# Optimization experiments

Measured on AMD Instinct MI355X. Metric: run time of the kernel, lower is better.

The kernel has to match this reference:

```python
import jax, jax.numpy as jnp
import numpy as np

GRID = 32
N_NODES = GRID * GRID          # 1024
PATCH = 1
C_IN = 3
NODE_F = C_IN * PATCH * PATCH  # 3
HID = 256
N_CLASSES = 10


def _build_norm_adj():
    # 5-point grid stencil + self loops, symmetrically normalized: D^-1/2 A D^-1/2
    adj = np.zeros((N_NODES, N_NODES), dtype=np.float32)
    idx = np.arange(N_NODES)
    i, j = idx // GRID, idx % GRID
    adj[idx, idx] = 1.0
    for di, dj in [(-1, 0), (1, 0), (0, -1), (0, 1)]:
        ni, nj = i + di, j + dj
        ok = (ni >= 0) & (ni < GRID) & (nj >= 0) & (nj < GRID)
        adj[idx[ok], (ni * GRID + nj)[ok]] = 1.0
    deg = adj.sum(axis=1)
    dis = np.where(deg > 0, deg ** -0.5, 0.0).astype(np.float32)
    return jnp.asarray(dis[:, None] * adj * dis[None, :])


def _image_to_graph(x):
    # [B,C,H,W] -> [B, grid, patch, grid, patch] blocks -> [B, N, C*patch^2]
    B = x.shape[0]
    x = x.reshape(B, C_IN, GRID, PATCH, GRID, PATCH)
    x = jnp.transpose(x, (0, 2, 4, 1, 3, 5))
    return x.reshape(B, N_NODES, NODE_F)


def setup_inputs() -> dict:
    key = jax.random.key(0)
    ks = jax.random.split(key, 10)
    s = 0.05
    return {
        "x": jax.random.normal(ks[0], (256, 3, 32, 32), dtype=jnp.float32),
        "W1": jax.random.normal(ks[1], (HID, NODE_F), dtype=jnp.float32) * s,
        "b1": jnp.zeros((HID,), dtype=jnp.float32),
        "W2": jax.random.normal(ks[2], (HID, HID), dtype=jnp.float32) * s,
        "b2": jnp.zeros((HID,), dtype=jnp.float32),
        "W3": jax.random.normal(ks[3], (HID // 2, HID), dtype=jnp.float32) * s,
        "b3": jnp.zeros((HID // 2,), dtype=jnp.float32),
        "Wc": jax.random.normal(ks[4], (N_CLASSES, N_NODES * (HID // 2)), dtype=jnp.float32) * s,
        "bc": jnp.zeros((N_CLASSES,), dtype=jnp.float32),
        "adj": _build_norm_adj(),
    }


def _gc(h, W, b, adj):
    # Linear, then fixed-adjacency aggregation, then ReLU
    h = jnp.einsum('bnf,hf->bnh', h, W) + b
    h = jnp.einsum('mn,bnh->bmh', adj, h)
    return jax.nn.relu(h)


def reference(x, W1, b1, W2, b2, W3, b3, Wc, bc, adj):
    h = _image_to_graph(x)                 # [B, N, 3]
    h = _gc(h, W1, b1, adj)                # [B, N, 256]
    h = _gc(h, W2, b2, adj)                # [B, N, 256]
    h = _gc(h, W3, b3, adj)                # [B, N, 128]
    h = h.reshape(h.shape[0], -1)          # [B, N*128]
    return h @ Wc.T + bc                   # [B, 10]
```

## Files before the change

### kernel.cpp

```cpp
#include <hip/hip_runtime.h>
#include <stdint.h>

#define N_NODES 1024
#define NCLS 10
#define KDIM 131072

typedef unsigned short u16;
typedef __bf16 bf16x8 __attribute__((ext_vector_type(8)));
typedef float f32x4 __attribute__((ext_vector_type(4)));
typedef float f32x2 __attribute__((ext_vector_type(2)));

__device__ __forceinline__ float b2f_lo(uint32_t u) {
  union { float f; uint32_t u; } v; v.u = u << 16; return v.f;
}
__device__ __forceinline__ float b2f_hi(uint32_t u) {
  union { float f; uint32_t u; } v; v.u = u & 0xFFFF0000u; return v.f;
}
__device__ __forceinline__ u16 f2b(float f) {
  union { float f; uint32_t u; } v; v.f = f;
  uint32_t r = v.u + 0x7FFF + ((v.u >> 16) & 1);
  return (u16)(r >> 16);
}
__device__ __forceinline__ uint32_t pkbf(float a, float b) {
#if __has_builtin(__builtin_amdgcn_cvt_pk_bf16_f32)
  typedef __bf16 bf2 __attribute__((ext_vector_type(2)));
  bf2 r = __builtin_amdgcn_cvt_pk_bf16_f32(a, b);
  union { bf2 v; uint32_t u; } c; c.v = r; return c.u;
#else
  union { float f; uint32_t u; } va, vb; va.f = a; vb.f = b;
  uint32_t ra = (va.u + 0x7FFF + ((va.u >> 16) & 1)) >> 16;
  uint32_t rb = (vb.u + 0x7FFF + ((vb.u >> 16) & 1)) & 0xFFFF0000u;
  return ra | rb;
#endif
}
__device__ __forceinline__ uint32_t pkbf2(f32x2 z) { return pkbf(z.x, z.y); }

__device__ __forceinline__ void async_copy16(const u16* g, u16* l) {
  __builtin_amdgcn_global_load_lds(
      (const __attribute__((address_space(1))) void*)g,
      (__attribute__((address_space(3))) void*)l, 16, 0, 0);
}

__device__ __forceinline__ void agg8p(uint4 v, float c, f32x2* acc) {
  const uint32_t* u = (const uint32_t*)&v;
  f32x2 cv = {c, c};
#pragma unroll
  for (int e = 0; e < 4; e++) {
    f32x2 p = {b2f_lo(u[e]), b2f_hi(u[e])};
    acc[e] += p * cv;
  }
}

__global__ __launch_bounds__(256) void cvt_w_kernel(const float* __restrict__ w,
                                                    u16* __restrict__ o, int n) {
  int i = blockIdx.x * 256 + threadIdx.x;
  if (i < n) o[i] = f2b(w[i]);
}

__global__ __launch_bounds__(256) void prep_wc_kernel(const float* __restrict__ wc,
                                                      u16* __restrict__ o) {
  int i = blockIdx.x * 256 + threadIdx.x;
  int row = i >> 17;
  int col = i & (KDIM - 1);
  o[i] = (row < NCLS) ? f2b(wc[row * KDIM + col]) : (u16)0;
}

__global__ __launch_bounds__(256) void prep_tab_kernel(const float* __restrict__ adj,
                                                       int* __restrict__ nbi,
                                                       float* __restrict__ nbc,
                                                       float* __restrict__ r) {
  int m = blockIdx.x * 256 + threadIdx.x;
  if (m >= N_NODES) return;
  int i = m >> 5, j = m & 31;
  const float* arow = adj + (size_t)m * N_NODES;
  int n[5]; float c[5];
  n[0] = m;                      c[0] = arow[m];
  n[1] = (i > 0)  ? m - 32 : m;  c[1] = (i > 0)  ? arow[m - 32] : 0.f;
  n[2] = (i < 31) ? m + 32 : m;  c[2] = (i < 31) ? arow[m + 32] : 0.f;
  n[3] = (j > 0)  ? m - 1  : m;  c[3] = (j > 0)  ? arow[m - 1]  : 0.f;
  n[4] = (j < 31) ? m + 1  : m;  c[4] = (j < 31) ? arow[m + 1]  : 0.f;
  float s = 0.f;
#pragma unroll
  for (int t = 0; t < 5; t++) { nbi[m * 5 + t] = n[t]; nbc[m * 5 + t] = c[t]; s += c[t]; }
  r[m] = s;
}

__global__ __launch_bounds__(256) void outinit_kernel(const float* __restrict__ bc,
                                                      float* __restrict__ out) {
  int idx = blockIdx.x * 256 + threadIdx.x;
  if (idx < 256 * NCLS) out[idx] = bc[idx % NCLS];
}

__global__ __launch_bounds__(256) void l1agg_kernel(
    const float* __restrict__ x,
    const float* __restrict__ W1,
    const float* __restrict__ b1,
    const int* __restrict__ nbi, const float* __restrict__ nbc,
    const float* __restrict__ r,
    u16* __restrict__ g)
{
  __shared__ u16 h1s[128 * 256];
  __shared__ float gxs[128][4];
  __shared__ float W1s[768];
  __shared__ float b1s[256];
  int p0 = blockIdx.x * 64;
  int b = p0 >> 10;
  int m0 = p0 & 1023;
  int e0 = m0 - 32;
  int tid = threadIdx.x;

  b1s[tid] = b1[tid];
  for (int i = tid; i < 768; i += 256) W1s[i] = W1[i];

  if (tid < 128) {
    int n = e0 + tid;
    float g0 = 0.f, g1 = 0.f, g2 = 0.f, rn = 0.f;
    if (n >= 0 && n < N_NODES) {
      const float* xb = x + (size_t)b * 3072;
#pragma unroll
      for (int t = 0; t < 5; t++) {
        int nb = nbi[n * 5 + t]; float cf = nbc[n * 5 + t];
        g0 += cf * xb[nb];
        g1 += cf * xb[1024 + nb];
        g2 += cf * xb[2048 + nb];
      }
      rn = r[n];
    }
    gxs[tid][0] = g0; gxs[tid][1] = g1; gxs[tid][2] = g2; gxs[tid][3] = rn;
  }
  __syncthreads();

  int ch8 = (tid & 31) * 8;
  f32x2 wp[3][4], bp[4];
#pragma unroll
  for (int p = 0; p < 4; p++) {
    int c = ch8 + 2 * p;
    wp[0][p] = (f32x2){W1s[c * 3],     W1s[(c + 1) * 3]};
    wp[1][p] = (f32x2){W1s[c * 3 + 1], W1s[(c + 1) * 3 + 1]};
    wp[2][p] = (f32x2){W1s[c * 3 + 2], W1s[(c + 1) * 3 + 2]};
    bp[p]    = (f32x2){b1s[c],         b1s[c + 1]};
  }

#pragma unroll
  for (int it = 0; it < 16; it++) {
    int node = (tid >> 5) + it * 8;
    f32x2 g0v = {gxs[node][0], gxs[node][0]};
    f32x2 g1v = {gxs[node][1], gxs[node][1]};
    f32x2 g2v = {gxs[node][2], gxs[node][2]};
    f32x2 rnv = {gxs[node][3], gxs[node][3]};
    uint32_t pk[4];
#pragma unroll
    for (int p = 0; p < 4; p++) {
      f32x2 z = g0v * wp[0][p] + g1v * wp[1][p] + g2v * wp[2][p] + rnv * bp[p];
      z.x = fmaxf(z.x, 0.f); z.y = fmaxf(z.y, 0.f);
      pk[p] = pkbf2(z);
    }
    *(uint4*)&h1s[node * 256 + ch8] = *(uint4*)pk;
  }
  __syncthreads();

#pragma unroll
  for (int it = 0; it < 8; it++) {
    int node = (tid >> 5) + it * 8;
    int m = m0 + node;
    f32x2 acc[4] = {};
#pragma unroll
    for (int t = 0; t < 5; t++) {
      int nb = nbi[m * 5 + t]; float cf = nbc[m * 5 + t];
      agg8p(*(const uint4*)&h1s[(nb - e0) * 256 + ch8], cf, acc);
    }
    uint4 o;
    o.x = pkbf2(acc[0]); o.y = pkbf2(acc[1]);
    o.z = pkbf2(acc[2]); o.w = pkbf2(acc[3]);
    *(uint4*)&g[(size_t)(p0 + node) * 256 + ch8] = o;
  }
}

__global__ __launch_bounds__(256, 4) void mm_kernel(
    const u16* __restrict__ A, const u16* __restrict__ W,
    const float* __restrict__ bias, const float* __restrict__ r,
    u16* __restrict__ C, int N)
{
  const int K = 256;
  __shared__ u16 As[2][128 * 32];
  __shared__ u16 Bs[2][128 * 32];
  int n0 = blockIdx.x * 128;
  int m0 = blockIdx.y * 128;
  int tid = threadIdx.x;
  int w = tid >> 6, l = tid & 63;
  int wm = w >> 1, wn = w & 1;

  int srow = w * 16 + (l >> 2);
  int skoff = (l & 3) * 8;
  const u16* ga0 = A + (size_t)(m0 + srow) * K + skoff;
  const u16* gb0 = W + (size_t)(n0 + srow) * K + skoff;

#define MM_ISSUE(kq, buf) \
  _Pragma("unroll") for (int q = 0; q < 2; q++) { \
    async_copy16(ga0 + (size_t)q * 64 * K + (kq) * 32, &As[buf][(q * 64 + w * 16) * 32]); \
    async_copy16(gb0 + (size_t)q * 64 * K + (kq) * 32, &Bs[buf][(q * 64 + w * 16) * 32]); \
  }

  MM_ISSUE(0, 0);

  f32x4 acc[4][4] = {};
  int lrow = l & 15, lq = l >> 4;

#pragma unroll
  for (int kq = 0; kq < 8; kq++) {
    int buf = kq & 1;
    __syncthreads();
    if (kq < 7) MM_ISSUE(kq + 1, buf ^ 1);
    const u16* pa = &As[buf][(wm * 64 + lrow) * 32 + lq * 8];
    const u16* pb = &Bs[buf][(wn * 64 + lrow) * 32 + lq * 8];
    bf16x8 af[4], bf[4];
#pragma unroll
    for (int t = 0; t < 4; t++) {
      af[t] = *(const bf16x8*)(pa + t * 16 * 32);
      bf[t] = *(const bf16x8*)(pb + t * 16 * 32);
    }
#pragma unroll
    for (int mt = 0; mt < 4; mt++)
#pragma unroll
      for (int nt = 0; nt < 4; nt++)
        acc[mt][nt] = __builtin_amdgcn_mfma_f32_16x16x32_bf16(af[mt], bf[nt], acc[mt][nt], 0, 0, 0);
  }
#undef MM_ISSUE

#pragma unroll
  for (int mt = 0; mt < 4; mt++)
#pragma unroll
    for (int nt = 0; nt < 4; nt++) {
      f32x4 v = acc[mt][nt];
      int col = n0 + wn * 64 + nt * 16 + lrow;
      float bs = bias[col];
#pragma unroll
      for (int i2 = 0; i2 < 4; i2++) {
        int row = m0 + wm * 64 + mt * 16 + lq * 4 + i2;
        float val = v[i2] + r[row & 1023] * bs;
        C[(size_t)row * N + col] = f2b(fmaxf(val, 0.f));
      }
    }
}

__global__ __launch_bounds__(256, 3) void mm3agg_kernel(
    const u16* __restrict__ H,
    const u16* __restrict__ W,
    const float* __restrict__ bias, const float* __restrict__ r,
    const int* __restrict__ nbi, const float* __restrict__ nbc,
    u16* __restrict__ C)
{
  const int K = 256, N = 128;
  const int AST = 40;
  __shared__ u16 As[2][128 * AST];
  __shared__ u16 Bs[2][128 * 32];
  int m0 = blockIdx.x * 128;
  int tid = threadIdx.x;
  int w = tid >> 6, l = tid & 63;
  int wm = w >> 1, wn = w & 1;

  int arow = tid >> 1;
  int acol = (tid & 1) * 16;
  int pg = m0 + arow;
  int node = pg & 1023;
  const u16* hb = H + ((size_t)(pg >> 10) << 10) * 256 + acol;
  const u16* nbp[5]; float cf[5];
#pragma unroll
  for (int j = 0; j < 5; j++) {
    nbp[j] = hb + (size_t)nbi[node * 5 + j] * 256;
    cf[j] = nbc[node * 5 + j];
  }

  int srow = w * 16 + (l >> 2);
  int skoff = (l & 3) * 8;
  const u16* gb0 = W + (size_t)srow * K + skoff;

#define M3_ISSUEB(kq, buf) \
  _Pragma("unroll") for (int q = 0; q < 2; q++) \
    async_copy16(gb0 + (size_t)q * 64 * K + (kq) * 32, &Bs[buf][(q * 64 + w * 16) * 32]);

#define M3_LOADA(kq) \
  _Pragma("unroll") for (int j = 0; j < 5; j++) \
    _Pragma("unroll") for (int q = 0; q < 2; q++) \
      L[j][q] = *(const uint4*)(nbp[j] + (kq) * 32 + q * 8);

#define M3_AGGSTORE(buf) { \
  u16* dst = &As[buf][arow * AST + acol]; \
  _Pragma("unroll") for (int q = 0; q < 2; q++) { \
    f32x2 a2[4] = {}; \
    _Pragma("unroll") for (int j = 0; j < 5; j++) agg8p(L[j][q], cf[j], a2); \
    uint4 o; \
    o.x = pkbf2(a2[0]); o.y = pkbf2(a2[1]); \
    o.z = pkbf2(a2[2]); o.w = pkbf2(a2[3]); \
    *(uint4*)(dst + q * 8) = o; \
  } }

  uint4 L[5][2];
  M3_ISSUEB(0, 0);
  M3_LOADA(0);
  M3_AGGSTORE(0);

  f32x4 acc[4][4] = {};
  int lrow = l & 15, lq = l >> 4;

#pragma unroll
  for (int kq = 0; kq < 8; kq++) {
    int buf = kq & 1;
    __syncthreads();
    if (kq < 7) {
      M3_ISSUEB(kq + 1, buf ^ 1);
      M3_LOADA(kq + 1);
    }
    const u16* pa = &As[buf][(wm * 64 + lrow) * AST + lq * 8];
    const u16* pb = &Bs[buf][(wn * 64 + lrow) * 32 + lq * 8];
    bf16x8 af[4], bf[4];
#pragma unroll
    for (int t = 0; t < 4; t++) {
      af[t] = *(const bf16x8*)(pa + t * 16 * AST);
      bf[t] = *(const bf16x8*)(pb + t * 16 * 32);
    }
#pragma unroll
    for (int mt = 0; mt < 4; mt++)
#pragma unroll
      for (int nt = 0; nt < 4; nt++)
        acc[mt][nt] = __builtin_amdgcn_mfma_f32_16x16x32_bf16(af[mt], bf[nt], acc[mt][nt], 0, 0, 0);
    if (kq < 7) M3_AGGSTORE(buf ^ 1);
  }
#undef M3_ISSUEB
#undef M3_LOADA
#undef M3_AGGSTORE

#pragma unroll
  for (int mt = 0; mt < 4; mt++)
#pragma unroll
    for (int nt = 0; nt < 4; nt++) {
      f32x4 v = acc[mt][nt];
      int col = wn * 64 + nt * 16 + lrow;
      float bs = bias[col];
#pragma unroll
      for (int i2 = 0; i2 < 4; i2++) {
        int row = m0 + wm * 64 + mt * 16 + lq * 4 + i2;
        float val = v[i2] + r[row & 1023] * bs;
        C[(size_t)row * N + col] = f2b(fmaxf(val, 0.f));
      }
    }
}

__global__ __launch_bounds__(256) void cls_kernel(
    const u16* __restrict__ h3,
    const u16* __restrict__ Wcb,
    float* __restrict__ out,
    int b0)
{
  int mt = blockIdx.x;
  int split = blockIdx.y;
  int w = threadIdx.x >> 6, l = threadIdx.x & 63;
  int lrow = l & 15, lq = l >> 4;
  f32x4 acc = {};
  int kbase = split * 4096 + w * 1024;
  const u16* pa = h3 + (size_t)(mt * 16 + lrow) * KDIM + kbase + lq * 8;
  const u16* pb = Wcb + (size_t)lrow * KDIM + kbase + lq * 8;
#pragma unroll 4
  for (int kk = 0; kk < 1024; kk += 32) {
    bf16x8 a = *(const bf16x8*)(pa + kk);
    bf16x8 b = *(const bf16x8*)(pb + kk);
    acc = __builtin_amdgcn_mfma_f32_16x16x32_bf16(a, b, acc, 0, 0, 0);
  }
  if (lrow < NCLS) {
#pragma unroll
    for (int i2 = 0; i2 < 4; i2++) {
      int b = b0 + mt * 16 + lq * 4 + i2;
      atomicAdd(&out[b * NCLS + lrow], acc[i2]);
    }
  }
}

extern "C" void kernel_launch(void* const* d_in, const int* in_sizes, int n_in,
                              void* d_out, int out_size, void* d_ws, size_t ws_size,
                              hipStream_t stream) {
  const float* x   = (const float*)d_in[0];
  const float* W1  = (const float*)d_in[1];
  const float* b1  = (const float*)d_in[2];
  const float* W2  = (const float*)d_in[3];
  const float* b2  = (const float*)d_in[4];
  const float* W3  = (const float*)d_in[5];
  const float* b3  = (const float*)d_in[6];
  const float* Wc  = (const float*)d_in[7];
  const float* bc  = (const float*)d_in[8];
  const float* adj = (const float*)d_in[9];
  float* out = (float*)d_out;
  const int B = 256;

  uint8_t* ws = (uint8_t*)d_ws;
  u16* W2b = (u16*)ws;  ws += (size_t)256 * 256 * 2;
  u16* W3b = (u16*)ws;  ws += (size_t)128 * 256 * 2;
  u16* Wcb = (u16*)ws;  ws += (size_t)16 * KDIM * 2;
  float* rr  = (float*)ws; ws += 1024 * 4;
  int*   nbi = (int*)ws;   ws += 1024 * 5 * 4;
  float* nbc = (float*)ws; ws += 1024 * 5 * 4;
  uintptr_t al = ((uintptr_t)ws + 255) & ~(uintptr_t)255;
  ws = (uint8_t*)al;
  size_t used = (size_t)(ws - (uint8_t*)d_ws);
  size_t avail = (ws_size > used) ? ws_size - used : 0;
  int chunk = 256;
  while (chunk > 32 && (size_t)chunk * 1024 * 256 * 2 * 2 > avail) chunk >>= 1;
  u16* bufA = (u16*)ws;
  u16* bufB = bufA + (size_t)chunk * 1024 * 256;

  cvt_w_kernel<<<256, 256, 0, stream>>>(W2, W2b, 256 * 256);
  cvt_w_kernel<<<128, 256, 0, stream>>>(W3, W3b, 128 * 256);
  prep_wc_kernel<<<(16 * KDIM) / 256, 256, 0, stream>>>(Wc, Wcb);
  prep_tab_kernel<<<4, 256, 0, stream>>>(adj, nbi, nbc, rr);
  outinit_kernel<<<(256 * NCLS + 255) / 256, 256, 0, stream>>>(bc, out);

  for (int b0 = 0; b0 < B; b0 += chunk) {
    const float* xb = x + (size_t)b0 * 3 * 1024;
    int M = chunk * 1024;
    l1agg_kernel<<<M / 64, 256, 0, stream>>>(xb, W1, b1, nbi, nbc, rr, bufB);
    {
      dim3 g(2, M / 128);
      mm_kernel<<<g, 256, 0, stream>>>(bufB, W2b, b2, rr, bufA, 256);
    }
    mm3agg_kernel<<<M / 128, 256, 0, stream>>>(bufA, W3b, b3, rr, nbi, nbc, bufB);
    dim3 gc(chunk / 16, 32);
    cls_kernel<<<gc, 256, 0, stream>>>(bufB, Wcb, out, b0);
  }
}
```

Measured before the change: 379.7 us.

## Stage full weight tile in swizzled LDS and stream A directly into registers

Both GEMM kernels now load the entire 128x256 weight tile into LDS once, using an XOR swizzle, in place of double-buffering 32-wide K slices of A and B. A operands are loaded straight from global memory into MFMA fragment registers, with a 3-deep register prefetch in mm_kernel and on-the-fly neighbour aggregation in mm3agg_kernel. This removes the per-K-step __syncthreads and the LDS round trip for A. In exchange the kernels use more LDS (64KB) and registers, the launch_bounds occupancy hints are dropped, and some global loads are redundant across the two wn warps.

```diff
diff --git a/kernel.cpp b/kernel.cpp
--- a/kernel.cpp
+++ b/kernel.cpp
@@ -176,48 +176,57 @@
   }
 }
 
-__global__ __launch_bounds__(256, 4) void mm_kernel(
+__global__ __launch_bounds__(256) void mm_kernel(
     const u16* __restrict__ A, const u16* __restrict__ W,
     const float* __restrict__ bias, const float* __restrict__ r,
     u16* __restrict__ C, int N)
 {
   const int K = 256;
-  __shared__ u16 As[2][128 * 32];
-  __shared__ u16 Bs[2][128 * 32];
+  __shared__ u16 Bs[128 * 256];
   int n0 = blockIdx.x * 128;
   int m0 = blockIdx.y * 128;
   int tid = threadIdx.x;
   int w = tid >> 6, l = tid & 63;
   int wm = w >> 1, wn = w & 1;
 
-  int srow = w * 16 + (l >> 2);
-  int skoff = (l & 3) * 8;
-  const u16* ga0 = A + (size_t)(m0 + srow) * K + skoff;
-  const u16* gb0 = W + (size_t)(n0 + srow) * K + skoff;
-
-#define MM_ISSUE(kq, buf) \
-  _Pragma("unroll") for (int q = 0; q < 2; q++) { \
-    async_copy16(ga0 + (size_t)q * 64 * K + (kq) * 32, &As[buf][(q * 64 + w * 16) * 32]); \
-    async_copy16(gb0 + (size_t)q * 64 * K + (kq) * 32, &Bs[buf][(q * 64 + w * 16) * 32]); \
-  }
-
-  MM_ISSUE(0, 0);
+  {
+    int r2 = l >> 5, poct = l & 31;
+#pragma unroll
+    for (int q = 0; q < 16; q++) {
+      int row = w * 32 + q * 2 + r2;
+      int loct = poct ^ (row & 7);
+      async_copy16(W + (size_t)(n0 + row) * K + loct * 8, &Bs[(w * 32 + q * 2) * 256]);
+    }
+  }
+
+  int lrow = l & 15, lq = l >> 4;
+  const u16* pa = A + (size_t)(m0 + wm * 64 + lrow) * K + lq * 8;
+
+  uint4 ab[3][4];
+#pragma unroll
+  for (int d = 0; d < 3; d++)
+#pragma unroll
+    for (int t = 0; t < 4; t++)
+      ab[d][t] = *(const uint4*)(pa + (size_t)t * 16 * K + d * 32);
 
   f32x4 acc[4][4] = {};
-  int lrow = l & 15, lq = l >> 4;
+  const u16* pb = &Bs[(wn * 64 + lrow) * 256];
+  int sw = lrow & 7;
+  __syncthreads();
 
 #pragma unroll
   for (int kq = 0; kq < 8; kq++) {
-    int buf = kq & 1;
-    __syncthreads();
-    if (kq < 7) MM_ISSUE(kq + 1, buf ^ 1);
-    const u16* pa = &As[buf][(wm * 64 + lrow) * 32 + lq * 8];
-    const u16* pb = &Bs[buf][(wn * 64 + lrow) * 32 + lq * 8];
     bf16x8 af[4], bf[4];
 #pragma unroll
     for (int t = 0; t < 4; t++) {
-      af[t] = *(const bf16x8*)(pa + t * 16 * 32);
-      bf[t] = *(const bf16x8*)(pb + t * 16 * 32);
+      union { uint4 u; bf16x8 b; } cv; cv.u = ab[kq % 3][t];
+      af[t] = cv.b;
+      bf[t] = *(const bf16x8*)(pb + t * 16 * 256 + ((kq * 4 + lq) ^ sw) * 8);
+    }
+    if (kq < 5) {
+#pragma unroll
+      for (int t = 0; t < 4; t++)
+        ab[kq % 3][t] = *(const uint4*)(pa + (size_t)t * 16 * K + (kq + 3) * 32);
     }
 #pragma unroll
     for (int mt = 0; mt < 4; mt++)
@@ -225,7 +234,6 @@
       for (int nt = 0; nt < 4; nt++)
         acc[mt][nt] = __builtin_amdgcn_mfma_f32_16x16x32_bf16(af[mt], bf[nt], acc[mt][nt], 0, 0, 0);
   }
-#undef MM_ISSUE
 
 #pragma unroll
   for (int mt = 0; mt < 4; mt++)
@@ -243,7 +251,7 @@
     }
 }
 
-__global__ __launch_bounds__(256, 3) void mm3agg_kernel(
+__global__ __launch_bounds__(256) void mm3agg_kernel(
     const u16* __restrict__ H,
     const u16* __restrict__ W,
     const float* __restrict__ bias, const float* __restrict__ r,
@@ -251,84 +259,64 @@
     u16* __restrict__ C)
 {
   const int K = 256, N = 128;
-  const int AST = 40;
-  __shared__ u16 As[2][128 * AST];
-  __shared__ u16 Bs[2][128 * 32];
+  __shared__ u16 Bs[128 * 256];
   int m0 = blockIdx.x * 128;
   int tid = threadIdx.x;
   int w = tid >> 6, l = tid & 63;
   int wm = w >> 1, wn = w & 1;
 
-  int arow = tid >> 1;
-  int acol = (tid & 1) * 16;
-  int pg = m0 + arow;
-  int node = pg & 1023;
-  const u16* hb = H + ((size_t)(pg >> 10) << 10) * 256 + acol;
-  const u16* nbp[5]; float cf[5];
-#pragma unroll
-  for (int j = 0; j < 5; j++) {
-    nbp[j] = hb + (size_t)nbi[node * 5 + j] * 256;
-    cf[j] = nbc[node * 5 + j];
-  }
-
-  int srow = w * 16 + (l >> 2);
-  int skoff = (l & 3) * 8;
-  const u16* gb0 = W + (size_t)srow * K + skoff;
-
-#define M3_ISSUEB(kq, buf) \
-  _Pragma("unroll") for (int q = 0; q < 2; q++) \
-    async_copy16(gb0 + (size_t)q * 64 * K + (kq) * 32, &Bs[buf][(q * 64 + w * 16) * 32]);
-
-#define M3_LOADA(kq) \
-  _Pragma("unroll") for (int j = 0; j < 5; j++) \
-    _Pragma("unroll") for (int q = 0; q < 2; q++) \
-      L[j][q] = *(const uint4*)(nbp[j] + (kq) * 32 + q * 8);
-
-#define M3_AGGSTORE(buf) { \
-  u16* dst = &As[buf][arow * AST + acol]; \
-  _Pragma("unroll") for (int q = 0; q < 2; q++) { \
-    f32x2 a2[4] = {}; \
-    _Pragma("unroll") for (int j = 0; j < 5; j++) agg8p(L[j][q], cf[j], a2); \
-    uint4 o; \
-    o.x = pkbf2(a2[0]); o.y = pkbf2(a2[1]); \
-    o.z = pkbf2(a2[2]); o.w = pkbf2(a2[3]); \
-    *(uint4*)(dst + q * 8) = o; \
-  } }
-
-  uint4 L[5][2];
-  M3_ISSUEB(0, 0);
-  M3_LOADA(0);
-  M3_AGGSTORE(0);
+  {
+    int r2 = l >> 5, poct = l & 31;
+#pragma unroll
+    for (int q = 0; q < 16; q++) {
+      int row = w * 32 + q * 2 + r2;
+      int loct = poct ^ (row & 7);
+      async_copy16(W + (size_t)row * K + loct * 8, &Bs[(w * 32 + q * 2) * 256]);
+    }
+  }
+
+  int lrow = l & 15, lq = l >> 4;
+  const u16* hb = H + ((size_t)(m0 >> 10) << 10) * 256 + lq * 8;
+  int offs[4][5]; float cf[4][5];
+#pragma unroll
+  for (int t = 0; t < 4; t++) {
+    int node = (m0 & 1023) + wm * 64 + t * 16 + lrow;
+#pragma unroll
+    for (int j = 0; j < 5; j++) {
+      offs[t][j] = nbi[node * 5 + j] * 256;
+      cf[t][j] = nbc[node * 5 + j];
+    }
+  }
 
   f32x4 acc[4][4] = {};
-  int lrow = l & 15, lq = l >> 4;
+  const u16* pb = &Bs[(wn * 64 + lrow) * 256];
+  int sw = lrow & 7;
+  __syncthreads();
 
 #pragma unroll
   for (int kq = 0; kq < 8; kq++) {
-    int buf = kq & 1;
-    __syncthreads();
-    if (kq < 7) {
-      M3_ISSUEB(kq + 1, buf ^ 1);
-      M3_LOADA(kq + 1);
-    }
-    const u16* pa = &As[buf][(wm * 64 + lrow) * AST + lq * 8];
-    const u16* pb = &Bs[buf][(wn * 64 + lrow) * 32 + lq * 8];
     bf16x8 af[4], bf[4];
 #pragma unroll
     for (int t = 0; t < 4; t++) {
-      af[t] = *(const bf16x8*)(pa + t * 16 * AST);
-      bf[t] = *(const bf16x8*)(pb + t * 16 * 32);
+      uint4 Lv[5];
+#pragma unroll
+      for (int j = 0; j < 5; j++)
+        Lv[j] = *(const uint4*)(hb + offs[t][j] + kq * 32);
+      f32x2 a2[4] = {};
+#pragma unroll
+      for (int j = 0; j < 5; j++) agg8p(Lv[j], cf[t][j], a2);
+      union { uint32_t u[4]; bf16x8 b; } cv;
+      cv.u[0] = pkbf2(a2[0]); cv.u[1] = pkbf2(a2[1]);
+      cv.u[2] = pkbf2(a2[2]); cv.u[3] = pkbf2(a2[3]);
+      af[t] = cv.b;
+      bf[t] = *(const bf16x8*)(pb + t * 16 * 256 + ((kq * 4 + lq) ^ sw) * 8);
     }
 #pragma unroll
     for (int mt = 0; mt < 4; mt++)
 #pragma unroll
       for (int nt = 0; nt < 4; nt++)
         acc[mt][nt] = __builtin_amdgcn_mfma_f32_16x16x32_bf16(af[mt], bf[nt], acc[mt][nt], 0, 0, 0);
-    if (kq < 7) M3_AGGSTORE(buf ^ 1);
-  }
-#undef M3_ISSUEB
-#undef M3_LOADA
-#undef M3_AGGSTORE
+  }
 
 #pragma unroll
   for (int mt = 0; mt < 4; mt++)
```

New measurement: 470.0 us. +23.8%, slower.

## Fuse classifier into layer-3 epilogue and retile layer-2 GEMM with swizzled LDS

Applied to the files above, without the earlier changes.

The classifier GEMM is folded into the mm3agg epilogue. Each thread multiplies its post-ReLU activations by a transposed bf16 Wc table laid out as [k][16], and a wave shuffle reduction feeds atomics into the output. This removes the h3 write and readback and the separate cls_kernel launch, at the cost of more per-element Wc gathers and atomics. The layer-2 GEMM is also retiled to 128x64 blocks with K-steps of 64 and an XOR-swizzled shared-memory layout, which doubles the grid and changes occupancy hints.

```diff
diff --git a/kernel.cpp b/kernel.cpp
--- a/kernel.cpp
+++ b/kernel.cpp
@@ -57,12 +57,12 @@
   if (i < n) o[i] = f2b(w[i]);
 }
 
-__global__ __launch_bounds__(256) void prep_wc_kernel(const float* __restrict__ wc,
-                                                      u16* __restrict__ o) {
+__global__ __launch_bounds__(256) void prep_wct_kernel(const float* __restrict__ wc,
+                                                       u16* __restrict__ o) {
   int i = blockIdx.x * 256 + threadIdx.x;
-  int row = i >> 17;
-  int col = i & (KDIM - 1);
-  o[i] = (row < NCLS) ? f2b(wc[row * KDIM + col]) : (u16)0;
+  int k = i >> 4;
+  int c = i & 15;
+  o[i] = (c < NCLS) ? f2b(wc[(size_t)c * KDIM + k]) : (u16)0;
 }
 
 __global__ __launch_bounds__(256) void prep_tab_kernel(const float* __restrict__ adj,
@@ -176,81 +176,86 @@
   }
 }
 
-__global__ __launch_bounds__(256, 4) void mm_kernel(
+__global__ __launch_bounds__(256) void mm_kernel(
     const u16* __restrict__ A, const u16* __restrict__ W,
     const float* __restrict__ bias, const float* __restrict__ r,
     u16* __restrict__ C, int N)
 {
   const int K = 256;
-  __shared__ u16 As[2][128 * 32];
-  __shared__ u16 Bs[2][128 * 32];
-  int n0 = blockIdx.x * 128;
+  __shared__ u16 As[2][128 * 64];
+  __shared__ u16 Bs[2][64 * 64];
+  int n0 = blockIdx.x * 64;
   int m0 = blockIdx.y * 128;
   int tid = threadIdx.x;
   int w = tid >> 6, l = tid & 63;
-  int wm = w >> 1, wn = w & 1;
-
-  int srow = w * 16 + (l >> 2);
-  int skoff = (l & 3) * 8;
-  const u16* ga0 = A + (size_t)(m0 + srow) * K + skoff;
-  const u16* gb0 = W + (size_t)(n0 + srow) * K + skoff;
+
+  int r8 = l >> 3, oct = l & 7;
+  int so = (oct ^ r8) << 3;
+  const u16* ga0 = A + (size_t)(m0 + w * 32 + r8) * K + so;
+  const u16* gb0 = W + (size_t)(n0 + w * 16 + r8) * K + so;
 
 #define MM_ISSUE(kq, buf) \
-  _Pragma("unroll") for (int q = 0; q < 2; q++) { \
-    async_copy16(ga0 + (size_t)q * 64 * K + (kq) * 32, &As[buf][(q * 64 + w * 16) * 32]); \
-    async_copy16(gb0 + (size_t)q * 64 * K + (kq) * 32, &Bs[buf][(q * 64 + w * 16) * 32]); \
-  }
+  _Pragma("unroll") for (int q = 0; q < 4; q++) \
+    async_copy16(ga0 + (size_t)q * 8 * K + (kq) * 64, &As[buf][(w * 32 + q * 8) * 64]); \
+  _Pragma("unroll") for (int q = 0; q < 2; q++) \
+    async_copy16(gb0 + (size_t)q * 8 * K + (kq) * 64, &Bs[buf][(w * 16 + q * 8) * 64]);
 
   MM_ISSUE(0, 0);
 
-  f32x4 acc[4][4] = {};
+  f32x4 acc[2][4] = {};
   int lrow = l & 15, lq = l >> 4;
-
-#pragma unroll
-  for (int kq = 0; kq < 8; kq++) {
+  int s = lrow & 7;
+
+#pragma unroll
+  for (int kq = 0; kq < 4; kq++) {
     int buf = kq & 1;
     __syncthreads();
-    if (kq < 7) MM_ISSUE(kq + 1, buf ^ 1);
-    const u16* pa = &As[buf][(wm * 64 + lrow) * 32 + lq * 8];
-    const u16* pb = &Bs[buf][(wn * 64 + lrow) * 32 + lq * 8];
-    bf16x8 af[4], bf[4];
-#pragma unroll
-    for (int t = 0; t < 4; t++) {
-      af[t] = *(const bf16x8*)(pa + t * 16 * 32);
-      bf[t] = *(const bf16x8*)(pb + t * 16 * 32);
-    }
-#pragma unroll
-    for (int mt = 0; mt < 4; mt++)
-#pragma unroll
-      for (int nt = 0; nt < 4; nt++)
-        acc[mt][nt] = __builtin_amdgcn_mfma_f32_16x16x32_bf16(af[mt], bf[nt], acc[mt][nt], 0, 0, 0);
+    if (kq < 3) { MM_ISSUE(kq + 1, buf ^ 1); }
+    const u16* pa = &As[buf][(w * 32 + lrow) * 64];
+    const u16* pb = &Bs[buf][lrow * 64];
+#pragma unroll
+    for (int kh = 0; kh < 2; kh++) {
+      int po = (((kh << 2) | lq) ^ s) << 3;
+      bf16x8 af[2], bf[4];
+#pragma unroll
+      for (int t = 0; t < 2; t++) af[t] = *(const bf16x8*)(pa + t * 16 * 64 + po);
+#pragma unroll
+      for (int t = 0; t < 4; t++) bf[t] = *(const bf16x8*)(pb + t * 16 * 64 + po);
+#pragma unroll
+      for (int mt = 0; mt < 2; mt++)
+#pragma unroll
+        for (int nt = 0; nt < 4; nt++)
+          acc[mt][nt] = __builtin_amdgcn_mfma_f32_16x16x32_bf16(af[mt], bf[nt], acc[mt][nt], 0, 0, 0);
+    }
   }
 #undef MM_ISSUE
 
 #pragma unroll
-  for (int mt = 0; mt < 4; mt++)
+  for (int mt = 0; mt < 2; mt++)
 #pragma unroll
     for (int nt = 0; nt < 4; nt++) {
       f32x4 v = acc[mt][nt];
-      int col = n0 + wn * 64 + nt * 16 + lrow;
+      int col = n0 + nt * 16 + lrow;
       float bs = bias[col];
 #pragma unroll
       for (int i2 = 0; i2 < 4; i2++) {
-        int row = m0 + wm * 64 + mt * 16 + lq * 4 + i2;
+        int row = m0 + w * 32 + mt * 16 + lq * 4 + i2;
         float val = v[i2] + r[row & 1023] * bs;
         C[(size_t)row * N + col] = f2b(fmaxf(val, 0.f));
       }
     }
 }
 
-__global__ __launch_bounds__(256, 3) void mm3agg_kernel(
+__global__ __launch_bounds__(256) void mm3agg_kernel(
     const u16* __restrict__ H,
     const u16* __restrict__ W,
     const float* __restrict__ bias, const float* __restrict__ r,
     const int* __restrict__ nbi, const float* __restrict__ nbc,
-    u16* __restrict__ C)
+    const u16* __restrict__ WcT,
+    float* __restrict__ out,
+    int b0)
 {
-  const int K = 256, N = 128;
+  const int K = 256;
   const int AST = 40;
   __shared__ u16 As[2][128 * AST];
   __shared__ u16 Bs[2][128 * 32];
@@ -262,13 +267,13 @@
   int arow = tid >> 1;
   int acol = (tid & 1) * 16;
   int pg = m0 + arow;
-  int node = pg & 1023;
+  int node0 = pg & 1023;
   const u16* hb = H + ((size_t)(pg >> 10) << 10) * 256 + acol;
   const u16* nbp[5]; float cf[5];
 #pragma unroll
   for (int j = 0; j < 5; j++) {
-    nbp[j] = hb + (size_t)nbi[node * 5 + j] * 256;
-    cf[j] = nbc[node * 5 + j];
+    nbp[j] = hb + (size_t)nbi[node0 * 5 + j] * 256;
+    cf[j] = nbc[node0 * 5 + j];
   }
 
   int srow = w * 16 + (l >> 2);
@@ -330,6 +335,7 @@
 #undef M3_LOADA
 #undef M3_AGGSTORE
 
+  f32x2 o5[5] = {};
 #pragma unroll
   for (int mt = 0; mt < 4; mt++)
 #pragma unroll
@@ -340,38 +346,33 @@
 #pragma unroll
       for (int i2 = 0; i2 < 4; i2++) {
         int row = m0 + wm * 64 + mt * 16 + lq * 4 + i2;
-        float val = v[i2] + r[row & 1023] * bs;
-        C[(size_t)row * N + col] = f2b(fmaxf(val, 0.f));
+        float val = fmaxf(v[i2] + r[row & 1023] * bs, 0.f);
+        const u16* wt = WcT + ((size_t)((row & 1023) * 128 + col) << 4);
+        uint4 wa = *(const uint4*)wt;
+        uint32_t wb = *(const uint32_t*)(wt + 8);
+        f32x2 vv = {val, val};
+        o5[0] += vv * (f32x2){b2f_lo(wa.x), b2f_hi(wa.x)};
+        o5[1] += vv * (f32x2){b2f_lo(wa.y), b2f_hi(wa.y)};
+        o5[2] += vv * (f32x2){b2f_lo(wa.z), b2f_hi(wa.z)};
+        o5[3] += vv * (f32x2){b2f_lo(wa.w), b2f_hi(wa.w)};
+        o5[4] += vv * (f32x2){b2f_lo(wb),   b2f_hi(wb)};
       }
     }
-}
-
-__global__ __launch_bounds__(256) void cls_kernel(
-    const u16* __restrict__ h3,
-    const u16* __restrict__ Wcb,
-    float* __restrict__ out,
-    int b0)
-{
-  int mt = blockIdx.x;
-  int split = blockIdx.y;
-  int w = threadIdx.x >> 6, l = threadIdx.x & 63;
-  int lrow = l & 15, lq = l >> 4;
-  f32x4 acc = {};
-  int kbase = split * 4096 + w * 1024;
-  const u16* pa = h3 + (size_t)(mt * 16 + lrow) * KDIM + kbase + lq * 8;
-  const u16* pb = Wcb + (size_t)lrow * KDIM + kbase + lq * 8;
-#pragma unroll 4
-  for (int kk = 0; kk < 1024; kk += 32) {
-    bf16x8 a = *(const bf16x8*)(pa + kk);
-    bf16x8 b = *(const bf16x8*)(pb + kk);
-    acc = __builtin_amdgcn_mfma_f32_16x16x32_bf16(a, b, acc, 0, 0, 0);
-  }
-  if (lrow < NCLS) {
-#pragma unroll
-    for (int i2 = 0; i2 < 4; i2++) {
-      int b = b0 + mt * 16 + lq * 4 + i2;
-      atomicAdd(&out[b * NCLS + lrow], acc[i2]);
-    }
+#pragma unroll
+  for (int off = 1; off < 64; off <<= 1) {
+#pragma unroll
+    for (int e = 0; e < 5; e++) {
+      o5[e].x += __shfl_xor(o5[e].x, off);
+      o5[e].y += __shfl_xor(o5[e].y, off);
+    }
+  }
+  if (l == 0) {
+    float* ob = out + (size_t)(b0 + (m0 >> 10)) * NCLS;
+    atomicAdd(ob + 0, o5[0].x); atomicAdd(ob + 1, o5[0].y);
+    atomicAdd(ob + 2, o5[1].x); atomicAdd(ob + 3, o5[1].y);
+    atomicAdd(ob + 4, o5[2].x); atomicAdd(ob + 5, o5[2].y);
+    atomicAdd(ob + 6, o5[3].x); atomicAdd(ob + 7, o5[3].y);
+    atomicAdd(ob + 8, o5[4].x); atomicAdd(ob + 9, o5[4].y);
   }
 }
 
@@ -394,7 +395,7 @@
   uint8_t* ws = (uint8_t*)d_ws;
   u16* W2b = (u16*)ws;  ws += (size_t)256 * 256 * 2;
   u16* W3b = (u16*)ws;  ws += (size_t)128 * 256 * 2;
-  u16* Wcb = (u16*)ws;  ws += (size_t)16 * KDIM * 2;
+  u16* WcT = (u16*)ws;  ws += (size_t)KDIM * 16 * 2;
   float* rr  = (float*)ws; ws += 1024 * 4;
   int*   nbi = (int*)ws;   ws += 1024 * 5 * 4;
   float* nbc = (float*)ws; ws += 1024 * 5 * 4;
@@ -409,7 +410,7 @@
 
   cvt_w_kernel<<<256, 256, 0, stream>>>(W2, W2b, 256 * 256);
   cvt_w_kernel<<<128, 256, 0, stream>>>(W3, W3b, 128 * 256);
-  prep_wc_kernel<<<(16 * KDIM) / 256, 256, 0, stream>>>(Wc, Wcb);
+  prep_wct_kernel<<<(KDIM * 16) / 256, 256, 0, stream>>>(Wc, WcT);
   prep_tab_kernel<<<4, 256, 0, stream>>>(adj, nbi, nbc, rr);
   outinit_kernel<<<(256 * NCLS + 255) / 256, 256, 0, stream>>>(bc, out);
 
@@ -418,11 +419,9 @@
     int M = chunk * 1024;
     l1agg_kernel<<<M / 64, 256, 0, stream>>>(xb, W1, b1, nbi, nbc, rr, bufB);
     {
-      dim3 g(2, M / 128);
+      dim3 g(4, M / 128);
       mm_kernel<<<g, 256, 0, stream>>>(bufB, W2b, b2, rr, bufA, 256);
     }
-    mm3agg_kernel<<<M / 128, 256, 0, stream>>>(bufA, W3b, b3, rr, nbi, nbc, bufB);
-    dim3 gc(chunk / 16, 32);
-    cls_kernel<<<gc, 256, 0, stream>>>(bufB, Wcb, out, b0);
-  }
-}
+    mm3agg_kernel<<<M / 128, 256, 0, stream>>>(bufA, W3b, b3, rr, nbi, nbc, WcT, out, b0);
+  }
+}
```

Result: slower. 433.8 us (+14.2%).

## Pre-swizzle weights into MFMA fragment layout and read B directly from global

Applied to the files above, without the earlier changes.

The weight preprocessing kernel now rearranges W2 and W3 into the per-lane MFMA fragment order, so the layer-2 and layer-3 GEMMs load B operands straight from global or cache with one 16-byte load per lane. This removes the B shared-memory staging and its async copies. The layer-2 GEMM also moves to a 64-wide K step with an XOR-swizzled A tile to avoid LDS bank conflicts and halve the number of barriers. In exchange, B loads now go through the cache hierarchy inside the MFMA loop rather than being prefetched, and the launch-bound occupancy hints are dropped.

```diff
diff --git a/kernel.cpp b/kernel.cpp
--- a/kernel.cpp
+++ b/kernel.cpp
@@ -51,10 +51,15 @@
   }
 }
 
-__global__ __launch_bounds__(256) void cvt_w_kernel(const float* __restrict__ w,
-                                                    u16* __restrict__ o, int n) {
+__global__ __launch_bounds__(256) void prep_wfrag_kernel(const float* __restrict__ w,
+                                                         u16* __restrict__ o, int n) {
   int i = blockIdx.x * 256 + threadIdx.x;
-  if (i < n) o[i] = f2b(w[i]);
+  if (i >= n) return;
+  int j = i & 7;
+  int l = (i >> 3) & 63;
+  int kq = (i >> 9) & 7;
+  int nt = i >> 12;
+  o[i] = f2b(w[(nt * 16 + (l & 15)) * 256 + kq * 32 + (l >> 4) * 8 + j]);
 }
 
 __global__ __launch_bounds__(256) void prep_wc_kernel(const float* __restrict__ wc,
@@ -176,54 +181,56 @@
   }
 }
 
-__global__ __launch_bounds__(256, 4) void mm_kernel(
-    const u16* __restrict__ A, const u16* __restrict__ W,
+__global__ __launch_bounds__(256) void mm_kernel(
+    const u16* __restrict__ A, const u16* __restrict__ Wf,
     const float* __restrict__ bias, const float* __restrict__ r,
     u16* __restrict__ C, int N)
 {
   const int K = 256;
-  __shared__ u16 As[2][128 * 32];
-  __shared__ u16 Bs[2][128 * 32];
+  __shared__ u16 As[2][128 * 64];
   int n0 = blockIdx.x * 128;
   int m0 = blockIdx.y * 128;
   int tid = threadIdx.x;
   int w = tid >> 6, l = tid & 63;
   int wm = w >> 1, wn = w & 1;
 
-  int srow = w * 16 + (l >> 2);
-  int skoff = (l & 3) * 8;
-  const u16* ga0 = A + (size_t)(m0 + srow) * K + skoff;
-  const u16* gb0 = W + (size_t)(n0 + srow) * K + skoff;
+  int r8 = l >> 3, oct = l & 7;
+  int so = (oct ^ r8) << 3;
+  const u16* ga0 = A + (size_t)(m0 + w * 32 + r8) * K + so;
 
 #define MM_ISSUE(kq, buf) \
-  _Pragma("unroll") for (int q = 0; q < 2; q++) { \
-    async_copy16(ga0 + (size_t)q * 64 * K + (kq) * 32, &As[buf][(q * 64 + w * 16) * 32]); \
-    async_copy16(gb0 + (size_t)q * 64 * K + (kq) * 32, &Bs[buf][(q * 64 + w * 16) * 32]); \
-  }
+  _Pragma("unroll") for (int q = 0; q < 4; q++) \
+    async_copy16(ga0 + (size_t)q * 8 * K + (kq) * 64, &As[buf][(w * 32 + q * 8) * 64]);
 
   MM_ISSUE(0, 0);
 
   f32x4 acc[4][4] = {};
   int lrow = l & 15, lq = l >> 4;
-
-#pragma unroll
-  for (int kq = 0; kq < 8; kq++) {
+  int s = lrow & 7;
+  const u16* wfb = Wf + (((size_t)(n0 >> 4) + wn * 4) * 8) * 512 + l * 8;
+
+#pragma unroll
+  for (int kq = 0; kq < 4; kq++) {
     int buf = kq & 1;
     __syncthreads();
-    if (kq < 7) MM_ISSUE(kq + 1, buf ^ 1);
-    const u16* pa = &As[buf][(wm * 64 + lrow) * 32 + lq * 8];
-    const u16* pb = &Bs[buf][(wn * 64 + lrow) * 32 + lq * 8];
-    bf16x8 af[4], bf[4];
-#pragma unroll
-    for (int t = 0; t < 4; t++) {
-      af[t] = *(const bf16x8*)(pa + t * 16 * 32);
-      bf[t] = *(const bf16x8*)(pb + t * 16 * 32);
-    }
-#pragma unroll
-    for (int mt = 0; mt < 4; mt++)
-#pragma unroll
-      for (int nt = 0; nt < 4; nt++)
-        acc[mt][nt] = __builtin_amdgcn_mfma_f32_16x16x32_bf16(af[mt], bf[nt], acc[mt][nt], 0, 0, 0);
+    if (kq < 3) { MM_ISSUE(kq + 1, buf ^ 1); }
+    const u16* pa = &As[buf][(wm * 64 + lrow) * 64];
+#pragma unroll
+    for (int kh = 0; kh < 2; kh++) {
+      int kk = kq * 2 + kh;
+      int po = (((kh << 2) | lq) ^ s) << 3;
+      bf16x8 af[4], bf[4];
+#pragma unroll
+      for (int t = 0; t < 4; t++) {
+        af[t] = *(const bf16x8*)(pa + t * 16 * 64 + po);
+        bf[t] = *(const bf16x8*)(wfb + ((size_t)t * 8 + kk) * 512);
+      }
+#pragma unroll
+      for (int mt = 0; mt < 4; mt++)
+#pragma unroll
+        for (int nt = 0; nt < 4; nt++)
+          acc[mt][nt] = __builtin_amdgcn_mfma_f32_16x16x32_bf16(af[mt], bf[nt], acc[mt][nt], 0, 0, 0);
+    }
   }
 #undef MM_ISSUE
 
@@ -243,17 +250,15 @@
     }
 }
 
-__global__ __launch_bounds__(256, 3) void mm3agg_kernel(
+__global__ __launch_bounds__(256) void mm3agg_kernel(
     const u16* __restrict__ H,
-    const u16* __restrict__ W,
+    const u16* __restrict__ W3f,
     const float* __restrict__ bias, const float* __restrict__ r,
     const int* __restrict__ nbi, const float* __restrict__ nbc,
     u16* __restrict__ C)
 {
-  const int K = 256, N = 128;
   const int AST = 40;
   __shared__ u16 As[2][128 * AST];
-  __shared__ u16 Bs[2][128 * 32];
   int m0 = blockIdx.x * 128;
   int tid = threadIdx.x;
   int w = tid >> 6, l = tid & 63;
@@ -262,22 +267,14 @@
   int arow = tid >> 1;
   int acol = (tid & 1) * 16;
   int pg = m0 + arow;
-  int node = pg & 1023;
+  int node0 = pg & 1023;
   const u16* hb = H + ((size_t)(pg >> 10) << 10) * 256 + acol;
   const u16* nbp[5]; float cf[5];
 #pragma unroll
   for (int j = 0; j < 5; j++) {
-    nbp[j] = hb + (size_t)nbi[node * 5 + j] * 256;
-    cf[j] = nbc[node * 5 + j];
-  }
-
-  int srow = w * 16 + (l >> 2);
-  int skoff = (l & 3) * 8;
-  const u16* gb0 = W + (size_t)srow * K + skoff;
-
-#define M3_ISSUEB(kq, buf) \
-  _Pragma("unroll") for (int q = 0; q < 2; q++) \
-    async_copy16(gb0 + (size_t)q * 64 * K + (kq) * 32, &Bs[buf][(q * 64 + w * 16) * 32]);
+    nbp[j] = hb + (size_t)nbi[node0 * 5 + j] * 256;
+    cf[j] = nbc[node0 * 5 + j];
+  }
 
 #define M3_LOADA(kq) \
   _Pragma("unroll") for (int j = 0; j < 5; j++) \
@@ -296,28 +293,24 @@
   } }
 
   uint4 L[5][2];
-  M3_ISSUEB(0, 0);
   M3_LOADA(0);
   M3_AGGSTORE(0);
 
   f32x4 acc[4][4] = {};
   int lrow = l & 15, lq = l >> 4;
+  const u16* wfb = W3f + ((size_t)wn * 4 * 8) * 512 + l * 8;
 
 #pragma unroll
   for (int kq = 0; kq < 8; kq++) {
     int buf = kq & 1;
     __syncthreads();
-    if (kq < 7) {
-      M3_ISSUEB(kq + 1, buf ^ 1);
-      M3_LOADA(kq + 1);
-    }
+    if (kq < 7) M3_LOADA(kq + 1);
     const u16* pa = &As[buf][(wm * 64 + lrow) * AST + lq * 8];
-    const u16* pb = &Bs[buf][(wn * 64 + lrow) * 32 + lq * 8];
     bf16x8 af[4], bf[4];
 #pragma unroll
     for (int t = 0; t < 4; t++) {
       af[t] = *(const bf16x8*)(pa + t * 16 * AST);
-      bf[t] = *(const bf16x8*)(pb + t * 16 * 32);
+      bf[t] = *(const bf16x8*)(wfb + ((size_t)t * 8 + kq) * 512);
     }
 #pragma unroll
     for (int mt = 0; mt < 4; mt++)
@@ -326,7 +319,6 @@
         acc[mt][nt] = __builtin_amdgcn_mfma_f32_16x16x32_bf16(af[mt], bf[nt], acc[mt][nt], 0, 0, 0);
     if (kq < 7) M3_AGGSTORE(buf ^ 1);
   }
-#undef M3_ISSUEB
 #undef M3_LOADA
 #undef M3_AGGSTORE
 
@@ -341,7 +333,7 @@
       for (int i2 = 0; i2 < 4; i2++) {
         int row = m0 + wm * 64 + mt * 16 + lq * 4 + i2;
         float val = v[i2] + r[row & 1023] * bs;
-        C[(size_t)row * N + col] = f2b(fmaxf(val, 0.f));
+        C[(size_t)row * 128 + col] = f2b(fmaxf(val, 0.f));
       }
     }
 }
@@ -392,8 +384,8 @@
   const int B = 256;
 
   uint8_t* ws = (uint8_t*)d_ws;
-  u16* W2b = (u16*)ws;  ws += (size_t)256 * 256 * 2;
-  u16* W3b = (u16*)ws;  ws += (size_t)128 * 256 * 2;
+  u16* W2f = (u16*)ws;  ws += (size_t)256 * 256 * 2;
+  u16* W3f = (u16*)ws;  ws += (size_t)128 * 256 * 2;
   u16* Wcb = (u16*)ws;  ws += (size_t)16 * KDIM * 2;
   float* rr  = (float*)ws; ws += 1024 * 4;
   int*   nbi = (int*)ws;   ws += 1024 * 5 * 4;
@@ -407,8 +399,8 @@
   u16* bufA = (u16*)ws;
   u16* bufB = bufA + (size_t)chunk * 1024 * 256;
 
-  cvt_w_kernel<<<256, 256, 0, stream>>>(W2, W2b, 256 * 256);
-  cvt_w_kernel<<<128, 256, 0, stream>>>(W3, W3b, 128 * 256);
+  prep_wfrag_kernel<<<256, 256, 0, stream>>>(W2, W2f, 256 * 256);
+  prep_wfrag_kernel<<<128, 256, 0, stream>>>(W3, W3f, 128 * 256);
   prep_wc_kernel<<<(16 * KDIM) / 256, 256, 0, stream>>>(Wc, Wcb);
   prep_tab_kernel<<<4, 256, 0, stream>>>(adj, nbi, nbc, rr);
   outinit_kernel<<<(256 * NCLS + 255) / 256, 256, 0, stream>>>(bc, out);
@@ -419,9 +411,9 @@
     l1agg_kernel<<<M / 64, 256, 0, stream>>>(xb, W1, b1, nbi, nbc, rr, bufB);
     {
       dim3 g(2, M / 128);
-      mm_kernel<<<g, 256, 0, stream>>>(bufB, W2b, b2, rr, bufA, 256);
-    }
-    mm3agg_kernel<<<M / 128, 256, 0, stream>>>(bufA, W3b, b3, rr, nbi, nbc, bufB);
+      mm_kernel<<<g, 256, 0, stream>>>(bufB, W2f, b2, rr, bufA, 256);
+    }
+    mm3agg_kernel<<<M / 128, 256, 0, stream>>>(bufA, W3f, b3, rr, nbi, nbc, bufB);
     dim3 gc(chunk / 16, 32);
     cls_kernel<<<gc, 256, 0, stream>>>(bufB, Wcb, out, b0);
   }
```

Measured after the change: 372.1 us. -2.0%, faster.
